# Performance work log

Hardware: AMD Instinct MI355X
Metric: run time of the kernel (lower is better)

Reference implementation:

```python
import jax, jax.numpy as jnp
import numpy as np

LEARNING_RATE = 0.005
WEIGHT_DECAY = 0.0001


def setup_inputs() -> dict:
    key = jax.random.key(0)
    k1, k2, k3 = jax.random.split(key, 3)
    B, POST, PRE = 128, 1024, 1024
    pre_spikes = jax.random.uniform(k1, (B, PRE), dtype=jnp.float32)
    post_spikes = jax.random.uniform(k2, (B, POST), dtype=jnp.float32)
    weights = jax.random.normal(k3, (POST, PRE), dtype=jnp.float32)
    return {"pre_spikes": pre_spikes, "post_spikes": post_spikes, "weights": weights}


def reference(pre_spikes, post_spikes, weights):
    # mean over batch of outer products post_b (x) pre_b == post^T @ pre / B
    B = pre_spikes.shape[0]
    mean_hebbian = jnp.einsum('bp,bq->pq', post_spikes, pre_spikes) / B  # (post, pre)
    dw = LEARNING_RATE * (mean_hebbian - WEIGHT_DECAY * weights)
    return dw
```

## Files before the change

### kernel.cpp

```cpp
#include <hip/hip_runtime.h>


using f32x16 = __attribute__((ext_vector_type(16))) float;
using short8 = __attribute__((ext_vector_type(8))) short;

constexpr int   N    = 1024;
constexpr int   K    = 128;
constexpr int   LSTR = 136;
constexpr float LR   = 0.005f;
constexpr float WD   = 0.0001f;

__device__ inline unsigned short f2bf(float x) {
    union { float f; unsigned int u; } c; c.f = x;
    return (unsigned short)((c.u + 0x7FFFu + ((c.u >> 16) & 1u)) >> 16);
}

__global__ __launch_bounds__(64) void hebb_mfma(
    const float* __restrict__ pre,
    const float* __restrict__ post,
    const float* __restrict__ W,
    float* __restrict__ out)
{
    __shared__ unsigned short A_lds[32 * LSTR];
    __shared__ unsigned short B_lds[32 * LSTR];

    const int l  = threadIdx.x;
    const int bm = blockIdx.y * 32;
    const int bn = blockIdx.x * 32;

    const int m4 = (l & 7) * 4;
    const int k8 = (l >> 3) * 8;

    #pragma unroll
    for (int p = 0; p < 2; ++p) {
        const int kb = k8 + p * 64;
        float4 av[8], bv[8];
        #pragma unroll
        for (int j = 0; j < 8; ++j) {
            av[j] = *(const float4*)(post + (size_t)(kb + j) * N + bm + m4);
            bv[j] = *(const float4*)(pre  + (size_t)(kb + j) * N + bn + m4);
        }
        #pragma unroll
        for (int i = 0; i < 4; ++i) {
            short8 pa, pb;
            #pragma unroll
            for (int j = 0; j < 8; ++j) {
                const float* fa = (const float*)&av[j];
                const float* fb = (const float*)&bv[j];
                pa[j] = (short)f2bf(fa[i]);
                pb[j] = (short)f2bf(fb[i]);
            }
            *(short8*)&A_lds[(m4 + i) * LSTR + kb] = pa;
            *(short8*)&B_lds[(m4 + i) * LSTR + kb] = pb;
        }
    }

    const int col   = l & 31;
    const int rbase = 4 * (l >> 5);
    float wv[16];
    #pragma unroll
    for (int r = 0; r < 16; ++r) {
        const int row = (r & 3) + 8 * (r >> 2) + rbase;
        wv[r] = W[(size_t)(bm + row) * N + bn + col];
    }

    __syncthreads();

    f32x16 acc = {};
    const int hh = 8 * (l >> 5);
    #pragma unroll
    for (int kk = 0; kk < 8; ++kk) {
        short8 a = *(const short8*)&A_lds[(l & 31) * LSTR + kk * 16 + hh];
        short8 b = *(const short8*)&B_lds[(l & 31) * LSTR + kk * 16 + hh];
        acc = __builtin_amdgcn_mfma_f32_32x32x16_bf16(a, b, acc, 0, 0, 0);
    }

    const float s1 = LR / 128.0f;
    const float s2 = LR * WD;
    #pragma unroll
    for (int r = 0; r < 16; ++r) {
        const int row = (r & 3) + 8 * (r >> 2) + rbase;
        out[(size_t)(bm + row) * N + bn + col] = s1 * acc[r] - s2 * wv[r];
    }
}

extern "C" void kernel_launch(void* const* d_in, const int* in_sizes, int n_in,
                              void* d_out, int out_size, void* d_ws, size_t ws_size,
                              hipStream_t stream) {
    const float* pre  = (const float*)d_in[0];
    const float* post = (const float*)d_in[1];
    const float* W    = (const float*)d_in[2];
    float* out = (float*)d_out;

    dim3 grid(N / 32, N / 32);
    dim3 block(64);
    hebb_mfma<<<grid, block, 0, stream>>>(pre, post, W, out);
}
```

Measured before the change: 63.06 us.

## Use 64x64 block tiles with four waves sharing bf16 operand panels in LDS

Each block now computes a 64x64 output tile with 256 threads (four waves, each doing a 32x32 MFMA tile) instead of a single wave per 32x32 tile. The A/B panels are loaded and converted to bf16 once per block and shared by two waves each, halving redundant global reads and conversion work for pre/post. The W load is also hoisted before the operand staging. The grid drops to 256 blocks, which on a 256-CU part means about one block per CU and less latency hiding from co-resident blocks.

```diff
diff --git a/kernel.cpp b/kernel.cpp
--- a/kernel.cpp
+++ b/kernel.cpp
@@ -5,7 +5,6 @@
 using short8 = __attribute__((ext_vector_type(8))) short;
 
 constexpr int   N    = 1024;
-constexpr int   K    = 128;
 constexpr int   LSTR = 136;
 constexpr float LR   = 0.005f;
 constexpr float WD   = 0.0001f;
@@ -15,53 +14,52 @@
     return (unsigned short)((c.u + 0x7FFFu + ((c.u >> 16) & 1u)) >> 16);
 }
 
-__global__ __launch_bounds__(64) void hebb_mfma(
+__global__ __launch_bounds__(256, 1) void hebb_mfma64(
     const float* __restrict__ pre,
     const float* __restrict__ post,
     const float* __restrict__ W,
     float* __restrict__ out)
 {
-    __shared__ unsigned short A_lds[32 * LSTR];
-    __shared__ unsigned short B_lds[32 * LSTR];
+    __shared__ unsigned short A_lds[64 * LSTR];
+    __shared__ unsigned short B_lds[64 * LSTR];
 
-    const int l  = threadIdx.x;
-    const int bm = blockIdx.y * 32;
-    const int bn = blockIdx.x * 32;
-
-    const int m4 = (l & 7) * 4;
-    const int k8 = (l >> 3) * 8;
-
-    #pragma unroll
-    for (int p = 0; p < 2; ++p) {
-        const int kb = k8 + p * 64;
-        float4 av[8], bv[8];
-        #pragma unroll
-        for (int j = 0; j < 8; ++j) {
-            av[j] = *(const float4*)(post + (size_t)(kb + j) * N + bm + m4);
-            bv[j] = *(const float4*)(pre  + (size_t)(kb + j) * N + bn + m4);
-        }
-        #pragma unroll
-        for (int i = 0; i < 4; ++i) {
-            short8 pa, pb;
-            #pragma unroll
-            for (int j = 0; j < 8; ++j) {
-                const float* fa = (const float*)&av[j];
-                const float* fb = (const float*)&bv[j];
-                pa[j] = (short)f2bf(fa[i]);
-                pb[j] = (short)f2bf(fb[i]);
-            }
-            *(short8*)&A_lds[(m4 + i) * LSTR + kb] = pa;
-            *(short8*)&B_lds[(m4 + i) * LSTR + kb] = pb;
-        }
-    }
+    const int tid = threadIdx.x;
+    const int l   = tid & 63;
+    const int w   = tid >> 6;
+    const int wr  = (w >> 1) * 32;
+    const int wc  = (w & 1) * 32;
+    const int bm  = blockIdx.y * 64;
+    const int bn  = blockIdx.x * 64;
 
     const int col   = l & 31;
     const int rbase = 4 * (l >> 5);
+
     float wv[16];
     #pragma unroll
     for (int r = 0; r < 16; ++r) {
         const int row = (r & 3) + 8 * (r >> 2) + rbase;
-        wv[r] = W[(size_t)(bm + row) * N + bn + col];
+        wv[r] = W[(size_t)(bm + wr + row) * N + bn + wc + col];
+    }
+
+    const int m4 = (tid & 15) * 4;
+    const int k8 = (tid >> 4) * 8;
+    float4 av[8], bv[8];
+    #pragma unroll
+    for (int j = 0; j < 8; ++j) {
+        av[j] = *(const float4*)(post + (size_t)(k8 + j) * N + bm + m4);
+        bv[j] = *(const float4*)(pre  + (size_t)(k8 + j) * N + bn + m4);
+    }
+
+    #pragma unroll
+    for (int i = 0; i < 4; ++i) {
+        short8 pa, pb;
+        #pragma unroll
+        for (int j = 0; j < 8; ++j) {
+            pa[j] = (short)f2bf(((const float*)&av[j])[i]);
+            pb[j] = (short)f2bf(((const float*)&bv[j])[i]);
+        }
+        *(short8*)&A_lds[(m4 + i) * LSTR + k8] = pa;
+        *(short8*)&B_lds[(m4 + i) * LSTR + k8] = pb;
     }
 
     __syncthreads();
@@ -70,8 +68,8 @@
     const int hh = 8 * (l >> 5);
     #pragma unroll
     for (int kk = 0; kk < 8; ++kk) {
-        short8 a = *(const short8*)&A_lds[(l & 31) * LSTR + kk * 16 + hh];
-        short8 b = *(const short8*)&B_lds[(l & 31) * LSTR + kk * 16 + hh];
+        short8 a = *(const short8*)&A_lds[(wr + (l & 31)) * LSTR + kk * 16 + hh];
+        short8 b = *(const short8*)&B_lds[(wc + (l & 31)) * LSTR + kk * 16 + hh];
         acc = __builtin_amdgcn_mfma_f32_32x32x16_bf16(a, b, acc, 0, 0, 0);
     }
 
@@ -80,7 +78,7 @@
     #pragma unroll
     for (int r = 0; r < 16; ++r) {
         const int row = (r & 3) + 8 * (r >> 2) + rbase;
-        out[(size_t)(bm + row) * N + bn + col] = s1 * acc[r] - s2 * wv[r];
+        out[(size_t)(bm + wr + row) * N + bn + wc + col] = s1 * acc[r] - s2 * wv[r];
     }
 }
 
@@ -92,7 +90,7 @@
     const float* W    = (const float*)d_in[2];
     float* out = (float*)d_out;
 
-    dim3 grid(N / 32, N / 32);
-    dim3 block(64);
-    hebb_mfma<<<grid, block, 0, stream>>>(pre, post, W, out);
+    dim3 grid(16, 16);
+    dim3 block(256);
+    hebb_mfma64<<<grid, block, 0, stream>>>(pre, post, W, out);
 }
```

Measured after the change: 62.08 us. No clear change (-1.5%).
